# Optimization experiments

Measured on AMD Instinct MI355X. Metric: run time of the kernel, lower is better.

## Reference

```python
import jax, jax.numpy as jnp
import numpy as np

N = 8192        # num_nodes
H = 128         # h_dim
E = 131072      # num edges (avg degree 16)
NREL = 90       # num relations
NB = 8          # num_bases (block-diagonal decomposition)
SI = H // NB    # block size 16


def setup_inputs() -> dict:
    key = jax.random.key(0)
    ks = jax.random.split(key, 24)
    sc = 0.01
    n = lambda k, shape, s=sc: jax.random.normal(k, shape, dtype=jnp.float32) * s
    return {
        'node_ids': jnp.arange(N, dtype=jnp.int32),
        'src': jax.random.randint(ks[0], (E,), 0, N, dtype=jnp.int32),
        'dst': jax.random.randint(ks[1], (E,), 0, N, dtype=jnp.int32),
        'etypes': jax.random.randint(ks[2], (E,), 0, NREL, dtype=jnp.int32),
        'norm': jax.random.uniform(ks[3], (E, 1), dtype=jnp.float32),
        'eps': jax.random.normal(ks[4], (N, H), dtype=jnp.float32),
        # input embedding layer
        'embedding': n(ks[5], (N, H)),
        # RelGraphConv layer 0 ('bdd'): per-relation block-diag weights, self-loop, bias
        'W0': n(ks[6], (NREL, NB, SI, SI)),
        'loop0': n(ks[7], (H, H)),
        'b0': jnp.zeros((H,), jnp.float32),
        # RelGraphConv layer 1
        'W1': n(ks[8], (NREL, NB, SI, SI)),
        'loop1': n(ks[9], (H, H)),
        'b1': jnp.zeros((H,), jnp.float32),
        # z_layer: Linear(H, 2H)  (weights stored as (in, out))
        'Wz': n(ks[10], (H, 2 * H)),
        'bz': jnp.zeros((2 * H,), jnp.float32),
        # inter_layer (UpdateLayer): Linear(H, H) + h_bias
        'Wi': n(ks[11], (H, H)),
        'bi': jnp.zeros((H,), jnp.float32),
        'hbi': jnp.zeros((H,), jnp.float32),
        # output_layer (second UpdateLayer)
        'Wo': n(ks[12], (H, H)),
        'bo': jnp.zeros((H,), jnp.float32),
        'hbo': jnp.zeros((H,), jnp.float32),
    }


def _rgcn_bdd(h, W, loop_w, bias, src, dst, etypes, norm, act):
    # gather src features, split into NB blocks of size SI
    x = h[src].reshape(-1, NB, SI)                       # [E, NB, SI]
    Wg = W[etypes]                                       # [E, NB, SI, SI] per-edge relation block weights
    msg = jnp.einsum('ebi,ebio->ebo', x, Wg).reshape(-1, H) * norm  # [E, H]
    agg = jax.ops.segment_sum(msg, dst, num_segments=N)  # scatter-add to dst
    out = agg + bias + h @ loop_w                        # self-loop + bias
    return act(out) if act is not None else out


def reference(node_ids, src, dst, etypes, norm, eps, embedding,
              W0, loop0, b0, W1, loop1, b1,
              Wz, bz, Wi, bi, hbi, Wo, bo, hbo):
    # input layer: embedding lookup; saved as input_embed
    x0 = embedding[node_ids]                             # [N, H]
    h = _rgcn_bdd(x0, W0, loop0, b0, src, dst, etypes, norm, jax.nn.relu)
    h = _rgcn_bdd(h, W1, loop1, b1, src, dst, etypes, norm, None)
    # VAE head: z ~ N(mean, exp(log_std))
    zml = h @ Wz + bz                                    # [N, 2H]
    z_mean, z_log_std = jnp.split(zml, 2, axis=-1)
    z = z_mean + jnp.exp(z_log_std) * eps                # reparameterized sample
    # decode 1: outer-product reconstruction + fused update
    R = z @ z.T                                          # [N, N]
    h = R @ (z @ Wi + bi) + R @ x0 + hbi
    # decode 2
    R2 = h @ h.T                                         # [N, N]
    out = R2 @ (h @ Wo + bo) + R2 @ x0 + hbo
    return out
```

## Files before the change

### kernel.cpp

```cpp
#include <hip/hip_runtime.h>
#include <hip/hip_bf16.h>
#include <math.h>

#define Hdim 128
#define NBq 8
#define SIq 16
#define LDP 136
#define SKX 64

typedef __attribute__((ext_vector_type(8))) short short8x;
typedef __attribute__((ext_vector_type(8))) _Float16 half8x;
typedef __attribute__((ext_vector_type(4))) float f32x4;
typedef __attribute__((ext_vector_type(4))) unsigned short ushort4x;
typedef __attribute__((ext_vector_type(2))) _Float16 half2x;

__device__ inline unsigned short f2b(float f) {
  unsigned int u = __float_as_uint(f);
  return (unsigned short)((u + 0x7fffu + ((u >> 16) & 1u)) >> 16);
}
__device__ inline unsigned int pack2(float lo, float hi) {
  return (unsigned int)f2b(lo) | ((unsigned int)f2b(hi) << 16);
}
__device__ inline unsigned short f2h(float f) {
  _Float16 h = (_Float16)f;
  unsigned short u;
  __builtin_memcpy(&u, &h, 2);
  return u;
}
__device__ inline half2x u2h(unsigned int u) {
  union { unsigned int u; half2x h; } v;
  v.u = u;
  return v.h;
}
__device__ inline float b2f(unsigned short u) {
  return __uint_as_float(((unsigned int)u) << 16);
}

__global__ __launch_bounds__(256) void k_pre(
    const float* __restrict__ emb, const int* __restrict__ ids, float* __restrict__ x0,
    unsigned short* __restrict__ x0h, unsigned short* __restrict__ x0t, int Nn,
    const float* __restrict__ W0, unsigned short* __restrict__ Wt0,
    const float* __restrict__ W1, unsigned short* __restrict__ Wt1, int w0elems,
    const float* __restrict__ l0, const float* __restrict__ l1,
    const float* __restrict__ Wi, const float* __restrict__ Wo, const float* __restrict__ Wz,
    unsigned short* __restrict__ l0t, unsigned short* __restrict__ l1t,
    unsigned short* __restrict__ Wit, unsigned short* __restrict__ Wot,
    unsigned short* __restrict__ Wzt,
    const int* __restrict__ dst, int* __restrict__ cnt, int E,
    int b1, int b2, int b3) {
  int bx = blockIdx.x, t = threadIdx.x;
  if (bx < b1) {
    int idx = bx * 256 + t;
    int n = idx >> 5, c4 = idx & 31;
    int s = ids[n];
    float4 v = ((const float4*)emb)[(size_t)s * 32 + c4];
    ((float4*)x0)[(size_t)n * 32 + c4] = v;
    ushort4x h;
    h.x = f2h(v.x); h.y = f2h(v.y); h.z = f2h(v.z); h.w = f2h(v.w);
    ((ushort4x*)x0h)[(size_t)n * 32 + c4] = h;
    int c0 = c4 * 4;
    x0t[(size_t)(c0 + 0) * Nn + n] = h.x;
    x0t[(size_t)(c0 + 1) * Nn + n] = h.y;
    x0t[(size_t)(c0 + 2) * Nn + n] = h.z;
    x0t[(size_t)(c0 + 3) * Nn + n] = h.w;
  } else if (bx < b2) {
    int idx = (bx - b1) * 256 + t;
    const float* W = (idx < w0elems) ? W0 : W1;
    unsigned short* Wt = (idx < w0elems) ? Wt0 : Wt1;
    int local = (idx < w0elems) ? idx : idx - w0elems;
    int rb = local >> 8, io = local & 255;
    int i = io >> 4, o = io & 15;
    Wt[(size_t)rb * 256 + o * 16 + i] = f2h(W[(size_t)rb * 256 + i * 16 + o]);
  } else if (bx < b3) {
    int idx = (bx - b2) * 256 + t;
    if (idx < 65536) {
      int w = idx >> 14, local = idx & 16383;
      const float* in = (w == 0) ? l0 : (w == 1) ? l1 : (w == 2) ? Wi : Wo;
      unsigned short* out = (w == 0) ? l0t : (w == 1) ? l1t : (w == 2) ? Wit : Wot;
      int n = local >> 7, k = local & 127;
      out[local] = f2b(in[k * 128 + n]);
    } else {
      int local = idx - 65536;
      int n = local >> 7, k = local & 127;
      Wzt[local] = f2b(Wz[k * 256 + n]);
    }
  } else {
    int e = (bx - b3) * 256 + t;
    if (e < E) atomicAdd(&cnt[dst[e]], 1);
  }
}

__global__ __launch_bounds__(1024) void k_scan(const int* __restrict__ cnt,
                                               int* __restrict__ off,
                                               int* __restrict__ cur, int N, int E) {
  __shared__ int part[1024];
  int t = threadIdx.x;
  int ipt = N / 1024;
  int base = t * ipt;
  int loc[8];
  int s = 0;
  for (int i = 0; i < ipt; ++i) { loc[i] = s; s += cnt[base + i]; }
  part[t] = s;
  __syncthreads();
  for (int d = 1; d < 1024; d <<= 1) {
    int v = part[t];
    int add = (t >= d) ? part[t - d] : 0;
    __syncthreads();
    part[t] = v + add;
    __syncthreads();
  }
  int pre = (t == 0) ? 0 : part[t - 1];
  for (int i = 0; i < ipt; ++i) {
    int o = pre + loc[i];
    off[base + i] = o;
    cur[base + i] = o;
  }
  if (t == 0) off[N] = E;
}

__global__ void k_scatter(const int* __restrict__ src, const int* __restrict__ dst,
                          const int* __restrict__ et, const float* __restrict__ norm,
                          int* __restrict__ cur, int4* __restrict__ pedge, int E) {
  int e = blockIdx.x * blockDim.x + threadIdx.x;
  if (e >= E) return;
  int p = atomicAdd(&cur[dst[e]], 1);
  pedge[p] = make_int4(src[e], et[e], __float_as_int(norm[e]), 0);
}

__global__ __launch_bounds__(128) void k_edge(
    const unsigned short* __restrict__ xh, const unsigned short* __restrict__ Wt,
    const int* __restrict__ off, const int4* __restrict__ pedge,
    float* __restrict__ agg) {
  int n = blockIdx.x;
  int f = threadIdx.x;
  int b = f >> 4, o = f & 15;
  int j0 = off[n], j1 = off[n + 1];
  float acc = 0.f;
#pragma unroll 2
  for (int j = j0; j < j1; ++j) {
    int4 meta = pedge[j];
    int s = meta.x;
    int r = meta.y;
    float nv = __int_as_float(meta.z);
    const uint4* xp = (const uint4*)(xh + (size_t)s * Hdim + b * SIq);
    const uint4* wp = (const uint4*)(Wt + ((size_t)r * NBq + b) * 256 + o * SIq);
    uint4 xa = xp[0], xc = xp[1];
    uint4 wa = wp[0], wc = wp[1];
#if __has_builtin(__builtin_amdgcn_fdot2)
    float d0 = 0.f, d1 = 0.f;
    d0 = __builtin_amdgcn_fdot2(u2h(xa.x), u2h(wa.x), d0, false);
    d1 = __builtin_amdgcn_fdot2(u2h(xa.y), u2h(wa.y), d1, false);
    d0 = __builtin_amdgcn_fdot2(u2h(xa.z), u2h(wa.z), d0, false);
    d1 = __builtin_amdgcn_fdot2(u2h(xa.w), u2h(wa.w), d1, false);
    d0 = __builtin_amdgcn_fdot2(u2h(xc.x), u2h(wc.x), d0, false);
    d1 = __builtin_amdgcn_fdot2(u2h(xc.y), u2h(wc.y), d1, false);
    d0 = __builtin_amdgcn_fdot2(u2h(xc.z), u2h(wc.z), d0, false);
    d1 = __builtin_amdgcn_fdot2(u2h(xc.w), u2h(wc.w), d1, false);
    acc = fmaf(d0 + d1, nv, acc);
#else
    float d = 0.f;
    unsigned int xu[8] = {xa.x, xa.y, xa.z, xa.w, xc.x, xc.y, xc.z, xc.w};
    unsigned int wu[8] = {wa.x, wa.y, wa.z, wa.w, wc.x, wc.y, wc.z, wc.w};
#pragma unroll
    for (int k = 0; k < 8; ++k) {
      half2x xv = u2h(xu[k]), wv = u2h(wu[k]);
      d += (float)xv.x * (float)wv.x + (float)xv.y * (float)wv.y;
    }
    acc = fmaf(d, nv, acc);
#endif
  }
  agg[(size_t)n * Hdim + f] = acc;
}

__global__ __launch_bounds__(256) void k_bgemm(
    const float* __restrict__ A, const unsigned short* __restrict__ Bt,
    float* __restrict__ C,
    const float* __restrict__ addm, const float* __restrict__ bias,
    int M, int Nc, int relu, unsigned short* __restrict__ Ch) {
  __shared__ unsigned short Al[32][136];
  __shared__ unsigned short Bl[64][136];
  int t = threadIdx.x;
  int bm = blockIdx.x * 32, bn = blockIdx.y * 64;
  {
    int r = t >> 3, c0 = (t & 7) << 4;
    const float4* ap = (const float4*)(A + (size_t)(bm + r) * Hdim + c0);
    float4 a0 = ap[0], a1 = ap[1], a2 = ap[2], a3 = ap[3];
    uint4 p0 = { pack2(a0.x, a0.y), pack2(a0.z, a0.w), pack2(a1.x, a1.y), pack2(a1.z, a1.w) };
    uint4 p1 = { pack2(a2.x, a2.y), pack2(a2.z, a2.w), pack2(a3.x, a3.y), pack2(a3.z, a3.w) };
    *(uint4*)&Al[r][c0]     = p0;
    *(uint4*)&Al[r][c0 + 8] = p1;
  }
  {
    int n = t >> 2, k0 = (t & 3) << 5;
    const uint4* bp = (const uint4*)(Bt + (size_t)(bn + n) * Hdim + k0);
    uint4 b0 = bp[0], b1 = bp[1], b2 = bp[2], b3 = bp[3];
    *(uint4*)&Bl[n][k0]      = b0;
    *(uint4*)&Bl[n][k0 + 8]  = b1;
    *(uint4*)&Bl[n][k0 + 16] = b2;
    *(uint4*)&Bl[n][k0 + 24] = b3;
  }
  __syncthreads();
  int wv = t >> 6, ln = t & 63;
  int mt = wv & 1;
  int nt0 = (wv >> 1) << 1;
  int lm = ln & 15, lk = ln >> 4;
  f32x4 acc0 = {0.f, 0.f, 0.f, 0.f}, acc1 = {0.f, 0.f, 0.f, 0.f};
#pragma unroll
  for (int ks = 0; ks < 4; ++ks) {
    short8x af = *(const short8x*)&Al[mt * 16 + lm][ks * 32 + lk * 8];
    short8x bf0 = *(const short8x*)&Bl[nt0 * 16 + lm][ks * 32 + lk * 8];
    short8x bf1 = *(const short8x*)&Bl[(nt0 + 1) * 16 + lm][ks * 32 + lk * 8];
    acc0 = __builtin_amdgcn_mfma_f32_16x16x32_bf16(af, bf0, acc0, 0, 0, 0);
    acc1 = __builtin_amdgcn_mfma_f32_16x16x32_bf16(af, bf1, acc1, 0, 0, 0);
  }
  int gcol0 = bn + nt0 * 16 + lm;
  int gcol1 = gcol0 + 16;
  float b0v = bias ? bias[gcol0] : 0.f;
  float b1v = bias ? bias[gcol1] : 0.f;
#pragma unroll
  for (int reg = 0; reg < 4; ++reg) {
    int grow = bm + mt * 16 + lk * 4 + reg;
    size_t o0 = (size_t)grow * Nc + gcol0;
    size_t o1 = (size_t)grow * Nc + gcol1;
    float v0 = acc0[reg] + b0v;
    float v1 = acc1[reg] + b1v;
    if (addm) { v0 += addm[o0]; v1 += addm[o1]; }
    if (relu) { v0 = fmaxf(v0, 0.f); v1 = fmaxf(v1, 0.f); }
    C[o0] = v0;
    C[o1] = v1;
    if (Ch) { Ch[o0] = f2h(v0); Ch[o1] = f2h(v1); }
  }
}

__global__ __launch_bounds__(256) void k_bgemm_z(
    const float* __restrict__ A, const unsigned short* __restrict__ Wzt,
    const float* __restrict__ bz, const float* __restrict__ eps,
    float* __restrict__ Z, int M, int Nn,
    unsigned short* __restrict__ Zth, float* __restrict__ gz) {
  __shared__ unsigned short Al[32][136];
  __shared__ unsigned short Bm[64][136];
  __shared__ unsigned short Bl[64][136];
  int t = threadIdx.x;
  int bm = blockIdx.x * 32, bn = blockIdx.y * 64;
  if (gz && blockIdx.x == 0 && blockIdx.y == 0 && t < 64)
    ((float4*)gz)[t] = make_float4(0.f, 0.f, 0.f, 0.f);
  {
    int r = t >> 3, c0 = (t & 7) << 4;
    const float4* ap = (const float4*)(A + (size_t)(bm + r) * Hdim + c0);
    float4 a0 = ap[0], a1 = ap[1], a2 = ap[2], a3 = ap[3];
    uint4 p0 = { pack2(a0.x, a0.y), pack2(a0.z, a0.w), pack2(a1.x, a1.y), pack2(a1.z, a1.w) };
    uint4 p1 = { pack2(a2.x, a2.y), pack2(a2.z, a2.w), pack2(a3.x, a3.y), pack2(a3.z, a3.w) };
    *(uint4*)&Al[r][c0]     = p0;
    *(uint4*)&Al[r][c0 + 8] = p1;
  }
  {
    int n = t >> 2, k0 = (t & 3) << 5;
    const uint4* mp = (const uint4*)(Wzt + (size_t)(bn + n) * Hdim + k0);
    const uint4* lp = (const uint4*)(Wzt + (size_t)(bn + 128 + n) * Hdim + k0);
    uint4 m0 = mp[0], m1 = mp[1], m2 = mp[2], m3 = mp[3];
    uint4 l0 = lp[0], l1 = lp[1], l2 = lp[2], l3 = lp[3];
    *(uint4*)&Bm[n][k0]      = m0; *(uint4*)&Bm[n][k0 + 8]  = m1;
    *(uint4*)&Bm[n][k0 + 16] = m2; *(uint4*)&Bm[n][k0 + 24] = m3;
    *(uint4*)&Bl[n][k0]      = l0; *(uint4*)&Bl[n][k0 + 8]  = l1;
    *(uint4*)&Bl[n][k0 + 16] = l2; *(uint4*)&Bl[n][k0 + 24] = l3;
  }
  __syncthreads();
  int wv = t >> 6, ln = t & 63;
  int mt = wv & 1;
  int nt0 = (wv >> 1) << 1;
  int lm = ln & 15, lk = ln >> 4;
  f32x4 am0 = {0,0,0,0}, am1 = {0,0,0,0}, al0 = {0,0,0,0}, al1 = {0,0,0,0};
#pragma unroll
  for (int ks = 0; ks < 4; ++ks) {
    short8x af = *(const short8x*)&Al[mt * 16 + lm][ks * 32 + lk * 8];
    short8x bm0 = *(const short8x*)&Bm[nt0 * 16 + lm][ks * 32 + lk * 8];
    short8x bm1 = *(const short8x*)&Bm[(nt0 + 1) * 16 + lm][ks * 32 + lk * 8];
    short8x bl0 = *(const short8x*)&Bl[nt0 * 16 + lm][ks * 32 + lk * 8];
    short8x bl1 = *(const short8x*)&Bl[(nt0 + 1) * 16 + lm][ks * 32 + lk * 8];
    am0 = __builtin_amdgcn_mfma_f32_16x16x32_bf16(af, bm0, am0, 0, 0, 0);
    am1 = __builtin_amdgcn_mfma_f32_16x16x32_bf16(af, bm1, am1, 0, 0, 0);
    al0 = __builtin_amdgcn_mfma_f32_16x16x32_bf16(af, bl0, al0, 0, 0, 0);
    al1 = __builtin_amdgcn_mfma_f32_16x16x32_bf16(af, bl1, al1, 0, 0, 0);
  }
  int gcol0 = bn + nt0 * 16 + lm;
  int gcol1 = gcol0 + 16;
  float bm0v = bz[gcol0], bm1v = bz[gcol1];
  float bl0v = bz[128 + gcol0], bl1v = bz[128 + gcol1];
#pragma unroll
  for (int reg = 0; reg < 4; ++reg) {
    int grow = bm + mt * 16 + lk * 4 + reg;
    size_t o0 = (size_t)grow * Hdim + gcol0;
    size_t o1 = (size_t)grow * Hdim + gcol1;
    float v0 = am0[reg] + bm0v + expf(al0[reg] + bl0v) * eps[o0];
    float v1 = am1[reg] + bm1v + expf(al1[reg] + bl1v) * eps[o1];
    Z[o0] = v0;
    Z[o1] = v1;
    Zth[(size_t)gcol0 * Nn + grow] = f2h(v0);
    Zth[(size_t)gcol1 * Nn + grow] = f2h(v1);
  }
}

__global__ __launch_bounds__(256) void k_xty2m(
    const unsigned short* __restrict__ Zt, const unsigned short* __restrict__ X0t,
    float* __restrict__ part, float* __restrict__ s1, float* __restrict__ cx0, int N) {
  int kc = blockIdx.x, yt = blockIdx.y;
  int t = threadIdx.x;
  int KC = N / SKX;
  int k0 = kc * KC;
  if (yt == 4) {
    int c = t & 127;
    const unsigned short* row = ((t >> 7) ? X0t : Zt) + (size_t)c * N + k0;
    float acc = 0.f;
    for (int i = 0; i < KC; i += 8) {
      uint4 v = *(const uint4*)(row + i);
      half2x a0 = u2h(v.x), a1 = u2h(v.y), a2 = u2h(v.z), a3 = u2h(v.w);
      acc += (float)a0.x + (float)a0.y + (float)a1.x + (float)a1.y
           + (float)a2.x + (float)a2.y + (float)a3.x + (float)a3.y;
    }
    atomicAdd(((t >> 7) ? cx0 : s1) + c, acc);
    return;
  }
  __shared__ unsigned short Asl[128][72];
  __shared__ unsigned short Bsl[64][72];
  int wv = t >> 6, ln = t & 63, lm = ln & 15, lk = ln >> 4;
  f32x4 acc[8];
#pragma unroll
  for (int i = 0; i < 8; ++i) acc[i] = (f32x4){0.f, 0.f, 0.f, 0.f};
  for (int ch = 0; ch < KC; ch += 64) {
    {
      int r = t >> 1, s = (t & 1) * 32;
      const uint4* gp = (const uint4*)(Zt + (size_t)r * N + k0 + ch + s);
      uint4 v0 = gp[0], v1 = gp[1], v2 = gp[2], v3 = gp[3];
      *(uint4*)&Asl[r][s]      = v0;
      *(uint4*)&Asl[r][s + 8]  = v1;
      *(uint4*)&Asl[r][s + 16] = v2;
      *(uint4*)&Asl[r][s + 24] = v3;
    }
    if (t < 128) {
      int n = t >> 1, s = (t & 1) * 32;
      int yn = yt * 64 + n;
      const unsigned short* Sb = (yn < 128) ? (Zt + (size_t)yn * N)
                                            : (X0t + (size_t)(yn - 128) * N);
      const uint4* gp = (const uint4*)(Sb + k0 + ch + s);
      uint4 v0 = gp[0], v1 = gp[1], v2 = gp[2], v3 = gp[3];
      *(uint4*)&Bsl[n][s]      = v0;
      *(uint4*)&Bsl[n][s + 8]  = v1;
      *(uint4*)&Bsl[n][s + 16] = v2;
      *(uint4*)&Bsl[n][s + 24] = v3;
    }
    __syncthreads();
#pragma unroll
    for (int ks = 0; ks < 2; ++ks) {
      half8x bf = *(const half8x*)&Bsl[wv * 16 + lm][ks * 32 + lk * 8];
#pragma unroll
      for (int mi = 0; mi < 8; ++mi) {
        half8x af = *(const half8x*)&Asl[mi * 16 + lm][ks * 32 + lk * 8];
        acc[mi] = __builtin_amdgcn_mfma_f32_16x16x32_f16(af, bf, acc[mi], 0, 0, 0);
      }
    }
    __syncthreads();
  }
  int gcol = yt * 64 + wv * 16 + lm;
  float* pb = part + (size_t)kc * (128 * 256) + gcol;
#pragma unroll
  for (int mi = 0; mi < 8; ++mi)
#pragma unroll
    for (int rg = 0; rg < 4; ++rg)
      pb[(size_t)(mi * 16 + lk * 4 + rg) * 256] = acc[mi][rg];
}

__global__ __launch_bounds__(256) void k_red(const float* __restrict__ part,
                                             float* __restrict__ SP) {
  int idx = blockIdx.x * 256 + threadIdx.x;
  float a = 0.f;
#pragma unroll 8
  for (int s = 0; s < SKX; ++s) a += part[(size_t)s * 32768 + idx];
  SP[idx] = a;
}

__device__ inline void stage_f32(unsigned short* dst, const float* __restrict__ src,
                                 int ldF, int t) {
#pragma unroll
  for (int it = 0; it < 2; ++it) {
    int id = it * 1024 + t; int row = id >> 4, ch = id & 15;
    const float4* gp = (const float4*)(src + (size_t)row * ldF) + ch * 2;
    float4 u = gp[0], v = gp[1];
    uint4 pk = { pack2(u.x, u.y), pack2(u.z, u.w), pack2(v.x, v.y), pack2(v.z, v.w) };
    *(uint4*)&dst[row * LDP + ch * 8] = pk;
  }
}
__device__ inline void stage_b16(unsigned short* dst, const unsigned short* __restrict__ src,
                                 int t) {
#pragma unroll
  for (int it = 0; it < 2; ++it) {
    int id = it * 1024 + t; int row = id >> 4, ch = id & 15;
    *(uint4*)&dst[row * LDP + ch * 8] = ((const uint4*)(src + (size_t)row * 128))[ch];
  }
}
__device__ inline void mm128(const unsigned short* A, const unsigned short* B,
                             f32x4 (&Cc)[2][2], int wr, int wc, int lm, int lk) {
#pragma unroll
  for (int ks = 0; ks < 4; ++ks) {
    short8x af0 = *(const short8x*)&A[(wr * 32 + lm) * LDP + ks * 32 + lk * 8];
    short8x af1 = *(const short8x*)&A[(wr * 32 + 16 + lm) * LDP + ks * 32 + lk * 8];
    short8x bf0 = *(const short8x*)&B[(wc * 32 + lm) * LDP + ks * 32 + lk * 8];
    short8x bf1 = *(const short8x*)&B[(wc * 32 + 16 + lm) * LDP + ks * 32 + lk * 8];
    Cc[0][0] = __builtin_amdgcn_mfma_f32_16x16x32_bf16(af0, bf0, Cc[0][0], 0, 0, 0);
    Cc[0][1] = __builtin_amdgcn_mfma_f32_16x16x32_bf16(af0, bf1, Cc[0][1], 0, 0, 0);
    Cc[1][0] = __builtin_amdgcn_mfma_f32_16x16x32_bf16(af1, bf0, Cc[1][0], 0, 0, 0);
    Cc[1][1] = __builtin_amdgcn_mfma_f32_16x16x32_bf16(af1, bf1, Cc[1][1], 0, 0, 0);
  }
}
#define ZEROC {                                           \
  _Pragma("unroll") for (int mi = 0; mi < 2; ++mi)        \
  _Pragma("unroll") for (int ni = 0; ni < 2; ++ni)        \
    C[mi][ni] = (f32x4){0.f, 0.f, 0.f, 0.f}; }

__global__ __launch_bounds__(1024) void k_fix(
    const float* __restrict__ SP, const float* __restrict__ s1g,
    const float* __restrict__ cx0g,
    const unsigned short* __restrict__ Wit, const unsigned short* __restrict__ Wot,
    const float* __restrict__ bi, const float* __restrict__ hbi,
    const float* __restrict__ bo, const float* __restrict__ hbo,
    unsigned short* __restrict__ G12t, float* __restrict__ bvec, float Nf) {
  __shared__ unsigned short T0[128 * LDP];
  __shared__ unsigned short T1[128 * LDP];
  __shared__ unsigned short T2[128 * LDP];
  __shared__ unsigned short T3[128 * LDP];
  __shared__ float s1l[128], tl[128], s2l[128], cxl[128], bil[128], bol[128], hl[128];
  int t = threadIdx.x;
  int wv = t >> 6, ln = t & 63, lm = ln & 15, lk = ln >> 4;
  int wr = wv >> 2, wc = wv & 3;
  if (t < 128) {
    s1l[t] = s1g[t]; cxl[t] = cx0g[t]; bil[t] = bi[t]; bol[t] = bo[t]; hl[t] = hbi[t];
  }
  stage_f32(T0, SP, 256, t);
  stage_b16(T1, Wit, t);
  __syncthreads();
  f32x4 C[2][2];
  ZEROC; mm128(T0, T1, C, wr, wc, lm, lk);
#pragma unroll
  for (int mi = 0; mi < 2; ++mi)
#pragma unroll
// ... 89 lines not shown
  for (int ni = 0; ni < 2; ++ni) {
    int gcol = wc * 32 + ni * 16 + lm;
    int g0 = wr * 32 + mi * 16 + lk * 4;
#pragma unroll
    for (int rg = 0; rg < 4; ++rg) {
      int grow = g0 + rg;
      g2v[mi][ni][rg] = C[mi][ni][rg] + s2l[grow] * bol[gcol]
                      + b2f(T0[grow * LDP + gcol]);
    }
  }
  __syncthreads();
#pragma unroll
  for (int mi = 0; mi < 2; ++mi)
#pragma unroll
  for (int ni = 0; ni < 2; ++ni) {
    int gcol = wc * 32 + ni * 16 + lm;
    int g0 = wr * 32 + mi * 16 + lk * 4;
    ushort4x pk;
#pragma unroll
    for (int rg = 0; rg < 4; ++rg) pk[rg] = f2b(g2v[mi][ni][rg]);
    *(ushort4x*)&T0[gcol * LDP + g0] = pk;
  }
  __syncthreads();
  {
    int row = t >> 3, seg = t & 7;
    const unsigned short* gr = T0 + row * LDP + seg * 16;
    float a2 = 0.f;
#pragma unroll
    for (int i = 0; i < 16; ++i) a2 += hl[seg * 16 + i] * b2f(gr[i]);
    a2 += __shfl_xor(a2, 1);
    a2 += __shfl_xor(a2, 2);
    a2 += __shfl_xor(a2, 4);
    if (seg == 0) bvec[row] = a2 + hbo[row];
  }
  ZEROC; mm128(T2, T0, C, wr, wc, lm, lk);
#pragma unroll
  for (int mi = 0; mi < 2; ++mi)
#pragma unroll
  for (int ni = 0; ni < 2; ++ni) {
    int gcol = wc * 32 + ni * 16 + lm;
    int g0 = wr * 32 + mi * 16 + lk * 4;
    ushort4x pk;
#pragma unroll
    for (int rg = 0; rg < 4; ++rg) pk[rg] = f2b(C[mi][ni][rg]);
    *(ushort4x*)&T1[gcol * LDP + g0] = pk;
  }
  __syncthreads();
#pragma unroll
  for (int it = 0; it < 2; ++it) {
    int id = it * 1024 + t; int row = id >> 4, ch = (id & 15) * 8;
    *(uint4*)&G12t[row * 128 + ch] = *(uint4*)&T1[row * LDP + ch];
  }
}

extern "C" void kernel_launch(void* const* d_in, const int* in_sizes, int n_in,
                              void* d_out, int out_size, void* d_ws, size_t ws_size,
                              hipStream_t stream) {
  const int*   node_ids = (const int*)d_in[0];
  const int*   src      = (const int*)d_in[1];
  const int*   dst      = (const int*)d_in[2];
  const int*   et       = (const int*)d_in[3];
  const float* norm     = (const float*)d_in[4];
  const float* eps      = (const float*)d_in[5];
  const float* emb      = (const float*)d_in[6];
  const float* W0       = (const float*)d_in[7];
  const float* loop0    = (const float*)d_in[8];
  const float* b0       = (const float*)d_in[9];
  const float* W1       = (const float*)d_in[10];
  const float* loop1    = (const float*)d_in[11];
  const float* b1       = (const float*)d_in[12];
  const float* Wz       = (const float*)d_in[13];
  const float* bz       = (const float*)d_in[14];
  const float* Wi       = (const float*)d_in[15];
  const float* bi       = (const float*)d_in[16];
  const float* hbi      = (const float*)d_in[17];
  const float* Wo       = (const float*)d_in[18];
  const float* bo       = (const float*)d_in[19];
  const float* hbo      = (const float*)d_in[20];
  float* out = (float*)d_out;

  const int N  = in_sizes[0];
  const int E  = in_sizes[1];
  const int RB = in_sizes[7] / (SIq * SIq);

  char* ws = (char*)d_ws;
  const size_t MB = 1u << 20;
  const size_t KB = 1u << 10;
  float* X0   = (float*)(ws + 0 * MB);
  float* B1p  = (float*)(ws + 4 * MB);
  float* B2p  = (float*)(ws + 8 * MB);
  float* AGG  = (float*)(ws + 12 * MB);
  float* part = (float*)(ws + 8 * MB);
  float* SPb  = (float*)(ws + 16 * MB);
  float* s1p  = SPb + 32768;
  float* cx0p = SPb + 32896;
  unsigned short* G12t = (unsigned short*)(ws + 16 * MB + 576 * KB);
  float* bvec = (float*)(ws + 16 * MB + 640 * KB);
  int*   offp = (int*)(ws + 17 * MB);
  int*   curp = (int*)(ws + 17 * MB + 128 * KB);
  int*   cntp = (int*)(ws + 17 * MB + 256 * KB);
  int4*  pedge = (int4*)(ws + 18 * MB);
  unsigned short* Wt0 = (unsigned short*)(ws + 20 * MB);
  unsigned short* Wt1 = (unsigned short*)(ws + 20 * MB + 512 * KB);
  unsigned short* l0t = (unsigned short*)(ws + 21 * MB);
  unsigned short* l1t = (unsigned short*)(ws + 21 * MB + 64 * KB);
  unsigned short* Wit = (unsigned short*)(ws + 21 * MB + 128 * KB);
  unsigned short* Wot = (unsigned short*)(ws + 21 * MB + 192 * KB);
  unsigned short* Wzt = (unsigned short*)(ws + 21 * MB + 256 * KB);
  unsigned short* X0H = (unsigned short*)(ws + 22 * MB);
  unsigned short* B1H = (unsigned short*)(ws + 24 * MB);
  unsigned short* Ztc = (unsigned short*)(ws + 26 * MB);
  unsigned short* X0t = (unsigned short*)(ws + 28 * MB);

  dim3 blk(256);

  const int w0elems = RB * 256;
  const int gB   = (N * 32) / 256;
  const int wtbB = (2 * w0elems + 255) / 256;
  const int wttB = 98304 / 256;
  const int histB = (E + 255) / 256;
  const int b1s = gB, b2s = gB + wtbB, b3s = gB + wtbB + wttB;
  hipMemsetAsync(cntp, 0, (size_t)N * sizeof(int), stream);
  k_pre<<<dim3(b3s + histB), blk, 0, stream>>>(
      emb, node_ids, X0, X0H, X0t, N, W0, Wt0, W1, Wt1, w0elems,
      loop0, loop1, Wi, Wo, Wz, l0t, l1t, Wit, Wot, Wzt,
      dst, cntp, E, b1s, b2s, b3s);
  k_scan<<<dim3(1), dim3(1024), 0, stream>>>(cntp, offp, curp, N, E);
  k_scatter<<<dim3((E + 255) / 256), blk, 0, stream>>>(src, dst, et, norm, curp, pedge, E);

  k_edge<<<dim3(N), dim3(128), 0, stream>>>(X0H, Wt0, offp, pedge, AGG);
  k_bgemm<<<dim3(N / 32, 2), blk, 0, stream>>>(X0, l0t, B1p, AGG, b0, N, Hdim, 1, B1H);
  k_edge<<<dim3(N), dim3(128), 0, stream>>>(B1H, Wt1, offp, pedge, AGG);
  k_bgemm<<<dim3(N / 32, 2), blk, 0, stream>>>(B1p, l1t, B2p, AGG, b1, N, Hdim, 0, nullptr);
  k_bgemm_z<<<dim3(N / 32, 2), blk, 0, stream>>>(B2p, Wzt, bz, eps, B1p, N, N, Ztc, s1p);
  k_xty2m<<<dim3(SKX, 5), blk, 0, stream>>>(Ztc, X0t, part, s1p, cx0p, N);
  k_red<<<dim3(128), blk, 0, stream>>>(part, SPb);
  k_fix<<<dim3(1), dim3(1024), 0, stream>>>(SPb, s1p, cx0p, Wit, Wot, bi, hbi, bo, hbo,
                                            G12t, bvec, (float)N);
  k_bgemm<<<dim3(N / 32, 2), blk, 0, stream>>>(B1p, G12t, out, nullptr, bvec, N, Hdim, 0, nullptr);
}
```

Measured before the change: 253.2 us.

## Drop transposed fp16 copies of Z and X0; transpose in shared memory instead

Removes the strided transposed writes of Z (in k_bgemm_z) and X0 (in k_pre) to separate column-major fp16 buffers. k_xty2m now reads row-major fp32 Z and fp16 X0 directly, converts to fp16 in registers and transposes while storing into shared memory. The column-sum path now also reads row-major with a per-element loop. This trades uncoalesced scattered global writes for scalar shared-memory transposed stores, possible bank conflicts, and reading fp32 Z (twice the bytes) in the Gram kernel. It also drops the trailing barrier by moving the sync before the shared stores.

Measured after the change: 261.1 us. 1.03x slower.

```diff
diff --git a/kernel.cpp b/kernel.cpp
--- a/kernel.cpp
+++ b/kernel.cpp
@@ -27,6 +27,11 @@
   __builtin_memcpy(&u, &h, 2);
   return u;
 }
+__device__ inline float h2f(unsigned short u) {
+  _Float16 h;
+  __builtin_memcpy(&h, &u, 2);
+  return (float)h;
+}
 __device__ inline half2x u2h(unsigned int u) {
   union { unsigned int u; half2x h; } v;
   v.u = u;
@@ -38,7 +43,7 @@
 
 __global__ __launch_bounds__(256) void k_pre(
     const float* __restrict__ emb, const int* __restrict__ ids, float* __restrict__ x0,
-    unsigned short* __restrict__ x0h, unsigned short* __restrict__ x0t, int Nn,
+    unsigned short* __restrict__ x0h,
     const float* __restrict__ W0, unsigned short* __restrict__ Wt0,
     const float* __restrict__ W1, unsigned short* __restrict__ Wt1, int w0elems,
     const float* __restrict__ l0, const float* __restrict__ l1,
@@ -58,11 +63,6 @@
     ushort4x h;
     h.x = f2h(v.x); h.y = f2h(v.y); h.z = f2h(v.z); h.w = f2h(v.w);
     ((ushort4x*)x0h)[(size_t)n * 32 + c4] = h;
-    int c0 = c4 * 4;
-    x0t[(size_t)(c0 + 0) * Nn + n] = h.x;
-    x0t[(size_t)(c0 + 1) * Nn + n] = h.y;
-    x0t[(size_t)(c0 + 2) * Nn + n] = h.z;
-    x0t[(size_t)(c0 + 3) * Nn + n] = h.w;
   } else if (bx < b2) {
     int idx = (bx - b1) * 256 + t;
     const float* W = (idx < w0elems) ? W0 : W1;
@@ -235,8 +235,7 @@
 __global__ __launch_bounds__(256) void k_bgemm_z(
     const float* __restrict__ A, const unsigned short* __restrict__ Wzt,
     const float* __restrict__ bz, const float* __restrict__ eps,
-    float* __restrict__ Z, int M, int Nn,
-    unsigned short* __restrict__ Zth, float* __restrict__ gz) {
+    float* __restrict__ Z, int M, float* __restrict__ gz) {
   __shared__ unsigned short Al[32][136];
   __shared__ unsigned short Bm[64][136];
   __shared__ unsigned short Bl[64][136];
@@ -291,17 +290,13 @@
     int grow = bm + mt * 16 + lk * 4 + reg;
     size_t o0 = (size_t)grow * Hdim + gcol0;
     size_t o1 = (size_t)grow * Hdim + gcol1;
-    float v0 = am0[reg] + bm0v + expf(al0[reg] + bl0v) * eps[o0];
-    float v1 = am1[reg] + bm1v + expf(al1[reg] + bl1v) * eps[o1];
-    Z[o0] = v0;
-    Z[o1] = v1;
-    Zth[(size_t)gcol0 * Nn + grow] = f2h(v0);
-    Zth[(size_t)gcol1 * Nn + grow] = f2h(v1);
+    Z[o0] = am0[reg] + bm0v + expf(al0[reg] + bl0v) * eps[o0];
+    Z[o1] = am1[reg] + bm1v + expf(al1[reg] + bl1v) * eps[o1];
   }
 }
 
 __global__ __launch_bounds__(256) void k_xty2m(
-    const unsigned short* __restrict__ Zt, const unsigned short* __restrict__ X0t,
+    const float* __restrict__ Z, const unsigned short* __restrict__ X0h,
     float* __restrict__ part, float* __restrict__ s1, float* __restrict__ cx0, int N) {
   int kc = blockIdx.x, yt = blockIdx.y;
   int t = threadIdx.x;
@@ -309,45 +304,63 @@
   int k0 = kc * KC;
   if (yt == 4) {
     int c = t & 127;
-    const unsigned short* row = ((t >> 7) ? X0t : Zt) + (size_t)c * N + k0;
     float acc = 0.f;
-    for (int i = 0; i < KC; i += 8) {
-      uint4 v = *(const uint4*)(row + i);
-      half2x a0 = u2h(v.x), a1 = u2h(v.y), a2 = u2h(v.z), a3 = u2h(v.w);
-      acc += (float)a0.x + (float)a0.y + (float)a1.x + (float)a1.y
-           + (float)a2.x + (float)a2.y + (float)a3.x + (float)a3.y;
-    }
-    atomicAdd(((t >> 7) ? cx0 : s1) + c, acc);
+    if (t >> 7) {
+      for (int i = 0; i < KC; ++i)
+        acc += h2f(X0h[(size_t)(k0 + i) * Hdim + c]);
+      atomicAdd(cx0 + c, acc);
+    } else {
+      for (int i = 0; i < KC; ++i)
+        acc += Z[(size_t)(k0 + i) * Hdim + c];
+      atomicAdd(s1 + c, acc);
+    }
     return;
   }
   __shared__ unsigned short Asl[128][72];
   __shared__ unsigned short Bsl[64][72];
   int wv = t >> 6, ln = t & 63, lm = ln & 15, lk = ln >> 4;
+  int sn = t & 63, sq = t >> 6;
   f32x4 acc[8];
 #pragma unroll
   for (int i = 0; i < 8; ++i) acc[i] = (f32x4){0.f, 0.f, 0.f, 0.f};
   for (int ch = 0; ch < KC; ch += 64) {
+    int nrow = k0 + ch + sn;
+    unsigned short atmp[32];
     {
-      int r = t >> 1, s = (t & 1) * 32;
-      const uint4* gp = (const uint4*)(Zt + (size_t)r * N + k0 + ch + s);
-      uint4 v0 = gp[0], v1 = gp[1], v2 = gp[2], v3 = gp[3];
-      *(uint4*)&Asl[r][s]      = v0;
-      *(uint4*)&Asl[r][s + 8]  = v1;
-      *(uint4*)&Asl[r][s + 16] = v2;
-      *(uint4*)&Asl[r][s + 24] = v3;
-    }
-    if (t < 128) {
-      int n = t >> 1, s = (t & 1) * 32;
-      int yn = yt * 64 + n;
-      const unsigned short* Sb = (yn < 128) ? (Zt + (size_t)yn * N)
-                                            : (X0t + (size_t)(yn - 128) * N);
-      const uint4* gp = (const uint4*)(Sb + k0 + ch + s);
-      uint4 v0 = gp[0], v1 = gp[1], v2 = gp[2], v3 = gp[3];
-      *(uint4*)&Bsl[n][s]      = v0;
-      *(uint4*)&Bsl[n][s + 8]  = v1;
-      *(uint4*)&Bsl[n][s + 16] = v2;
-      *(uint4*)&Bsl[n][s + 24] = v3;
-    }
+      const float4* zr = (const float4*)(Z + (size_t)nrow * Hdim + sq * 32);
+#pragma unroll
+      for (int u = 0; u < 8; ++u) {
+        float4 v = zr[u];
+        atmp[u * 4 + 0] = f2h(v.x);
+        atmp[u * 4 + 1] = f2h(v.y);
+        atmp[u * 4 + 2] = f2h(v.z);
+        atmp[u * 4 + 3] = f2h(v.w);
+      }
+    }
+    unsigned short btmp[16];
+    if (yt < 2) {
+      const float4* zr = (const float4*)(Z + (size_t)nrow * Hdim + yt * 64 + sq * 16);
+#pragma unroll
+      for (int u = 0; u < 4; ++u) {
+        float4 v = zr[u];
+        btmp[u * 4 + 0] = f2h(v.x);
+        btmp[u * 4 + 1] = f2h(v.y);
+        btmp[u * 4 + 2] = f2h(v.z);
+        btmp[u * 4 + 3] = f2h(v.w);
+      }
+    } else {
+      const uint4* xr = (const uint4*)(X0h + (size_t)nrow * Hdim + (yt - 2) * 64 + sq * 16);
+#pragma unroll
+      for (int u = 0; u < 2; ++u) {
+        uint4 v = xr[u];
+        __builtin_memcpy(&btmp[u * 8], &v, 16);
+      }
+    }
+    __syncthreads();
+#pragma unroll
+    for (int q = 0; q < 32; ++q) Asl[sq * 32 + q][sn] = atmp[q];
+#pragma unroll
+    for (int q = 0; q < 16; ++q) Bsl[sq * 16 + q][sn] = btmp[q];
     __syncthreads();
 #pragma unroll
     for (int ks = 0; ks < 2; ++ks) {
@@ -358,7 +371,6 @@
         acc[mi] = __builtin_amdgcn_mfma_f32_16x16x32_f16(af, bf, acc[mi], 0, 0, 0);
       }
     }
-    __syncthreads();
   }
   int gcol = yt * 64 + wv * 16 + lm;
   float* pb = part + (size_t)kc * (128 * 256) + gcol;
@@ -641,8 +653,6 @@
   unsigned short* Wzt = (unsigned short*)(ws + 21 * MB + 256 * KB);
   unsigned short* X0H = (unsigned short*)(ws + 22 * MB);
   unsigned short* B1H = (unsigned short*)(ws + 24 * MB);
-  unsigned short* Ztc = (unsigned short*)(ws + 26 * MB);
-  unsigned short* X0t = (unsigned short*)(ws + 28 * MB);
 
   dim3 blk(256);
 
@@ -654,7 +664,7 @@
   const int b1s = gB, b2s = gB + wtbB, b3s = gB + wtbB + wttB;
   hipMemsetAsync(cntp, 0, (size_t)N * sizeof(int), stream);
   k_pre<<<dim3(b3s + histB), blk, 0, stream>>>(
-      emb, node_ids, X0, X0H, X0t, N, W0, Wt0, W1, Wt1, w0elems,
+      emb, node_ids, X0, X0H, W0, Wt0, W1, Wt1, w0elems,
       loop0, loop1, Wi, Wo, Wz, l0t, l1t, Wit, Wot, Wzt,
       dst, cntp, E, b1s, b2s, b3s);
   k_scan<<<dim3(1), dim3(1024), 0, stream>>>(cntp, offp, curp, N, E);
@@ -664,8 +674,8 @@
   k_bgemm<<<dim3(N / 32, 2), blk, 0, stream>>>(X0, l0t, B1p, AGG, b0, N, Hdim, 1, B1H);
   k_edge<<<dim3(N), dim3(128), 0, stream>>>(B1H, Wt1, offp, pedge, AGG);
   k_bgemm<<<dim3(N / 32, 2), blk, 0, stream>>>(B1p, l1t, B2p, AGG, b1, N, Hdim, 0, nullptr);
-  k_bgemm_z<<<dim3(N / 32, 2), blk, 0, stream>>>(B2p, Wzt, bz, eps, B1p, N, N, Ztc, s1p);
-  k_xty2m<<<dim3(SKX, 5), blk, 0, stream>>>(Ztc, X0t, part, s1p, cx0p, N);
+  k_bgemm_z<<<dim3(N / 32, 2), blk, 0, stream>>>(B2p, Wzt, bz, eps, B1p, N, s1p);
+  k_xty2m<<<dim3(SKX, 5), blk, 0, stream>>>(B1p, X0H, part, s1p, cx0p, N);
   k_red<<<dim3(128), blk, 0, stream>>>(part, SPb);
   k_fix<<<dim3(1), dim3(1024), 0, stream>>>(SPb, s1p, cx0p, Wit, Wot, bi, hbi, bo, hbo,
                                             G12t, bvec, (float)N);
```

## Group edges by relation and compute messages with MFMA, then segment-reduce

Applied to the files above, without the earlier changes.

Edges are now bucketed by relation type via a second histogram and scan, so 16-edge tiles of the same relation can run the block-diagonal transform as a 16x16x32 f16 MFMA. Each message is scaled by its norm and written as fp16 into a per-edge buffer indexed by its dst-sorted slot. A separate kernel then sums each node's contiguous messages. This replaces the per-edge scalar dot-product loop, which reloaded relation weights for every edge. In exchange it adds an extra E×H fp16 round trip through global memory, more atomics in the scatter stage, and fp16 rounding of every message.

New measurement: 538.6 us. 2.13x slower.

```diff
diff --git a/kernel.cpp b/kernel.cpp
--- a/kernel.cpp
+++ b/kernel.cpp
@@ -46,7 +46,8 @@
     unsigned short* __restrict__ l0t, unsigned short* __restrict__ l1t,
     unsigned short* __restrict__ Wit, unsigned short* __restrict__ Wot,
     unsigned short* __restrict__ Wzt,
-    const int* __restrict__ dst, int* __restrict__ cnt, int E,
+    const int* __restrict__ dst, const int* __restrict__ et,
+    int* __restrict__ cnt, int* __restrict__ ehist, int E,
     int b1, int b2, int b3) {
   int bx = blockIdx.x, t = threadIdx.x;
   if (bx < b1) {
@@ -86,13 +87,20 @@
     }
   } else {
     int e = (bx - b3) * 256 + t;
-    if (e < E) atomicAdd(&cnt[dst[e]], 1);
+    if (e < E) {
+      atomicAdd(&cnt[dst[e]], 1);
+      atomicAdd(&ehist[et[e]], 1);
+    }
   }
 }
 
 __global__ __launch_bounds__(1024) void k_scan(const int* __restrict__ cnt,
                                                int* __restrict__ off,
-                                               int* __restrict__ cur, int N, int E) {
+                                               int* __restrict__ cur, int N, int E,
+                                               const int* __restrict__ ehist,
+                                               int* __restrict__ eoff,
+                                               int* __restrict__ ecur,
+                                               int* __restrict__ tileoff, int NREL) {
   __shared__ int part[1024];
   int t = threadIdx.x;
   int ipt = N / 1024;
@@ -115,61 +123,97 @@
     off[base + i] = o;
     cur[base + i] = o;
   }
-  if (t == 0) off[N] = E;
+  if (t == 0) {
+    off[N] = E;
+    int run = 0, trun = 0;
+    for (int r = 0; r < NREL; ++r) {
+      eoff[r] = run; ecur[r] = run; tileoff[r] = trun;
+      int c = ehist[r];
+      run += c; trun += (c + 15) >> 4;
+    }
+    eoff[NREL] = run; tileoff[NREL] = trun;
+  }
 }
 
 __global__ void k_scatter(const int* __restrict__ src, const int* __restrict__ dst,
                           const int* __restrict__ et, const float* __restrict__ norm,
-                          int* __restrict__ cur, int4* __restrict__ pedge, int E) {
+                          int* __restrict__ cur, int* __restrict__ ecur,
+                          int4* __restrict__ pedge, int E) {
   int e = blockIdx.x * blockDim.x + threadIdx.x;
   if (e >= E) return;
   int p = atomicAdd(&cur[dst[e]], 1);
-  pedge[p] = make_int4(src[e], et[e], __float_as_int(norm[e]), 0);
-}
-
-__global__ __launch_bounds__(128) void k_edge(
-    const unsigned short* __restrict__ xh, const unsigned short* __restrict__ Wt,
-    const int* __restrict__ off, const int4* __restrict__ pedge,
-    float* __restrict__ agg) {
-  int n = blockIdx.x;
-  int f = threadIdx.x;
-  int b = f >> 4, o = f & 15;
+  int q = atomicAdd(&ecur[et[e]], 1);
+  pedge[q] = make_int4(src[e], p, __float_as_int(norm[e]), 0);
+}
+
+__global__ __launch_bounds__(256) void k_msg(
+    const unsigned short* __restrict__ xh,
+    const unsigned short* __restrict__ Wt,
+    const int4* __restrict__ em,
+    const int* __restrict__ eoff, const int* __restrict__ tileoff,
+    unsigned short* __restrict__ msg, int NREL) {
+  __shared__ int toff[128];
+  int t = threadIdx.x;
+  if (t <= NREL) toff[t] = tileoff[t];
+  __syncthreads();
+  int ntiles = toff[NREL];
+  int l = t & 63, w = t >> 6;
+  int lm = l & 15, lg = l >> 4;
+#pragma unroll 1
+  for (int tt = 0; tt < 4; ++tt) {
+    int tile = blockIdx.x * 4 + tt;
+    if (tile >= ntiles) break;
+    int lo = 0, hi = NREL - 1;
+    while (lo < hi) { int mid = (lo + hi + 1) >> 1; if (toff[mid] <= tile) lo = mid; else hi = mid - 1; }
+    int r = lo;
+    int estart = eoff[r] + (tile - toff[r]) * 16;
+    int count = eoff[r + 1] - estart;
+    if (count > 16) count = 16;
+    int4 meta = em[estart + (lm < count ? lm : 0)];
+    int msrc = meta.x;
+#pragma unroll
+    for (int bb = 0; bb < 2; ++bb) {
+      int b = w + bb * 4;
+      half8x af;
+#pragma unroll
+      for (int j = 0; j < 8; ++j) af[j] = (_Float16)0.f;
+      if (lg < 2 && lm < count)
+        af = *(const half8x*)(xh + (size_t)msrc * Hdim + b * 16 + lg * 8);
+      int gg = lg & 1;
+      half8x bf = *(const half8x*)(Wt + ((size_t)r * NBq + b) * 256 + lm * 16 + gg * 8);
+      f32x4 d = {0.f, 0.f, 0.f, 0.f};
+      d = __builtin_amdgcn_mfma_f32_16x16x32_f16(af, bf, d, 0, 0, 0);
+#pragma unroll
+      for (int reg = 0; reg < 4; ++reg) {
+        int m2 = lg * 4 + reg;
+        int slot = __shfl(meta.y, m2);
+        int nb2  = __shfl(meta.z, m2);
+        if (m2 < count)
+          msg[(size_t)slot * Hdim + b * 16 + lm] = f2h(d[reg] * __int_as_float(nb2));
+      }
+    }
+  }
+}
+
+__global__ __launch_bounds__(256) void k_seg(const unsigned short* __restrict__ msg,
+                                             const int* __restrict__ off,
+                                             float* __restrict__ agg) {
+  int n = blockIdx.x * 16 + (threadIdx.x >> 4);
+  int c8 = (threadIdx.x & 15) * 8;
   int j0 = off[n], j1 = off[n + 1];
-  float acc = 0.f;
-#pragma unroll 2
+  float acc[8] = {0.f, 0.f, 0.f, 0.f, 0.f, 0.f, 0.f, 0.f};
   for (int j = j0; j < j1; ++j) {
-    int4 meta = pedge[j];
-    int s = meta.x;
-    int r = meta.y;
-    float nv = __int_as_float(meta.z);
-    const uint4* xp = (const uint4*)(xh + (size_t)s * Hdim + b * SIq);
-    const uint4* wp = (const uint4*)(Wt + ((size_t)r * NBq + b) * 256 + o * SIq);
-    uint4 xa = xp[0], xc = xp[1];
-    uint4 wa = wp[0], wc = wp[1];
-#if __has_builtin(__builtin_amdgcn_fdot2)
-    float d0 = 0.f, d1 = 0.f;
-    d0 = __builtin_amdgcn_fdot2(u2h(xa.x), u2h(wa.x), d0, false);
-    d1 = __builtin_amdgcn_fdot2(u2h(xa.y), u2h(wa.y), d1, false);
-    d0 = __builtin_amdgcn_fdot2(u2h(xa.z), u2h(wa.z), d0, false);
-    d1 = __builtin_amdgcn_fdot2(u2h(xa.w), u2h(wa.w), d1, false);
-    d0 = __builtin_amdgcn_fdot2(u2h(xc.x), u2h(wc.x), d0, false);
-    d1 = __builtin_amdgcn_fdot2(u2h(xc.y), u2h(wc.y), d1, false);
-    d0 = __builtin_amdgcn_fdot2(u2h(xc.z), u2h(wc.z), d0, false);
-    d1 = __builtin_amdgcn_fdot2(u2h(xc.w), u2h(wc.w), d1, false);
-    acc = fmaf(d0 + d1, nv, acc);
-#else
-    float d = 0.f;
-    unsigned int xu[8] = {xa.x, xa.y, xa.z, xa.w, xc.x, xc.y, xc.z, xc.w};
-    unsigned int wu[8] = {wa.x, wa.y, wa.z, wa.w, wc.x, wc.y, wc.z, wc.w};
-#pragma unroll
-    for (int k = 0; k < 8; ++k) {
-      half2x xv = u2h(xu[k]), wv = u2h(wu[k]);
-      d += (float)xv.x * (float)wv.x + (float)xv.y * (float)wv.y;
-    }
-    acc = fmaf(d, nv, acc);
-#endif
-  }
-  agg[(size_t)n * Hdim + f] = acc;
+    uint4 v = *(const uint4*)(msg + (size_t)j * Hdim + c8);
+    half2x h0 = u2h(v.x), h1 = u2h(v.y), h2 = u2h(v.z), h3 = u2h(v.w);
+    acc[0] += (float)h0.x; acc[1] += (float)h0.y;
+    acc[2] += (float)h1.x; acc[3] += (float)h1.y;
+    acc[4] += (float)h2.x; acc[5] += (float)h2.y;
+    acc[6] += (float)h3.x; acc[7] += (float)h3.y;
+  }
+  float4 o0 = {acc[0], acc[1], acc[2], acc[3]};
+  float4 o1 = {acc[4], acc[5], acc[6], acc[7]};
+  *(float4*)(agg + (size_t)n * Hdim + c8)     = o0;
+  *(float4*)(agg + (size_t)n * Hdim + c8 + 4) = o1;
 }
 
 __global__ __launch_bounds__(256) void k_bgemm(
@@ -614,6 +658,7 @@
   const int N  = in_sizes[0];
   const int E  = in_sizes[1];
   const int RB = in_sizes[7] / (SIq * SIq);
+  const int NREL = RB / NBq;
 
   char* ws = (char*)d_ws;
   const size_t MB = 1u << 20;
@@ -631,6 +676,10 @@
   int*   offp = (int*)(ws + 17 * MB);
   int*   curp = (int*)(ws + 17 * MB + 128 * KB);
   int*   cntp = (int*)(ws + 17 * MB + 256 * KB);
+  int*   ehist = cntp + N;
+  int*   eoffp = (int*)(ws + 17 * MB + 320 * KB);
+  int*   ecurp = (int*)(ws + 17 * MB + 328 * KB);
+  int*   tilep = (int*)(ws + 17 * MB + 336 * KB);
   int4*  pedge = (int4*)(ws + 18 * MB);
   unsigned short* Wt0 = (unsigned short*)(ws + 20 * MB);
   unsigned short* Wt1 = (unsigned short*)(ws + 20 * MB + 512 * KB);
@@ -643,6 +692,7 @@
   unsigned short* B1H = (unsigned short*)(ws + 24 * MB);
   unsigned short* Ztc = (unsigned short*)(ws + 26 * MB);
   unsigned short* X0t = (unsigned short*)(ws + 28 * MB);
+  unsigned short* msg = (unsigned short*)(ws + 32 * MB);
 
   dim3 blk(256);
 
@@ -652,17 +702,24 @@
   const int wttB = 98304 / 256;
   const int histB = (E + 255) / 256;
   const int b1s = gB, b2s = gB + wtbB, b3s = gB + wtbB + wttB;
-  hipMemsetAsync(cntp, 0, (size_t)N * sizeof(int), stream);
+  hipMemsetAsync(cntp, 0, (size_t)(N + 128) * sizeof(int), stream);
   k_pre<<<dim3(b3s + histB), blk, 0, stream>>>(
       emb, node_ids, X0, X0H, X0t, N, W0, Wt0, W1, Wt1, w0elems,
       loop0, loop1, Wi, Wo, Wz, l0t, l1t, Wit, Wot, Wzt,
-      dst, cntp, E, b1s, b2s, b3s);
-  k_scan<<<dim3(1), dim3(1024), 0, stream>>>(cntp, offp, curp, N, E);
-  k_scatter<<<dim3((E + 255) / 256), blk, 0, stream>>>(src, dst, et, norm, curp, pedge, E);
-
-  k_edge<<<dim3(N), dim3(128), 0, stream>>>(X0H, Wt0, offp, pedge, AGG);
+      dst, et, cntp, ehist, E, b1s, b2s, b3s);
+  k_scan<<<dim3(1), dim3(1024), 0, stream>>>(cntp, offp, curp, N, E,
+                                             ehist, eoffp, ecurp, tilep, NREL);
+  k_scatter<<<dim3((E + 255) / 256), blk, 0, stream>>>(src, dst, et, norm, curp,
+                                                       ecurp, pedge, E);
+
+  const int maxTiles = E / 16 + NREL;
+  const int msgB = (maxTiles + 3) / 4;
+
+  k_msg<<<dim3(msgB), blk, 0, stream>>>(X0H, Wt0, pedge, eoffp, tilep, msg, NREL);
+  k_seg<<<dim3(N / 16), blk, 0, stream>>>(msg, offp, AGG);
   k_bgemm<<<dim3(N / 32, 2), blk, 0, stream>>>(X0, l0t, B1p, AGG, b0, N, Hdim, 1, B1H);
-  k_edge<<<dim3(N), dim3(128), 0, stream>>>(B1H, Wt1, offp, pedge, AGG);
+  k_msg<<<dim3(msgB), blk, 0, stream>>>(B1H, Wt1, pedge, eoffp, tilep, msg, NREL);
+  k_seg<<<dim3(N / 16), blk, 0, stream>>>(msg, offp, AGG);
   k_bgemm<<<dim3(N / 32, 2), blk, 0, stream>>>(B1p, l1t, B2p, AGG, b1, N, Hdim, 0, nullptr);
   k_bgemm_z<<<dim3(N / 32, 2), blk, 0, stream>>>(B2p, Wzt, bz, eps, B1p, N, N, Ztc, s1p);
   k_xty2m<<<dim3(SKX, 5), blk, 0, stream>>>(Ztc, X0t, part, s1p, cx0p, N);
```

## Fuse edge message aggregation into self-loop GEMM kernel

Applied to the files above, without the earlier changes.

Merges the per-node edge gather/aggregate kernel into the self-loop bf16 MFMA GEMM, so each 32x64 tile computes its aggregation into shared memory and adds it in the epilogue. This removes two kernel launches per layer and the global round-trip of the AGG buffer. In exchange the grid shrinks from N blocks of 128 threads to N/32 x 2 blocks, each looping over 8 nodes per wave serially, which may lower the parallelism available for hiding gather latency.

New measurement: 291.9 us. 1.15x slower.

```diff
diff --git a/kernel.cpp b/kernel.cpp
--- a/kernel.cpp
+++ b/kernel.cpp
@@ -127,49 +127,114 @@
   pedge[p] = make_int4(src[e], et[e], __float_as_int(norm[e]), 0);
 }
 
-__global__ __launch_bounds__(128) void k_edge(
+__global__ __launch_bounds__(256) void k_bgemm_e(
+    const float* __restrict__ A, const unsigned short* __restrict__ Bt,
+    float* __restrict__ C, const float* __restrict__ bias,
+    int M, int relu, unsigned short* __restrict__ Ch,
     const unsigned short* __restrict__ xh, const unsigned short* __restrict__ Wt,
-    const int* __restrict__ off, const int4* __restrict__ pedge,
-    float* __restrict__ agg) {
-  int n = blockIdx.x;
-  int f = threadIdx.x;
-  int b = f >> 4, o = f & 15;
-  int j0 = off[n], j1 = off[n + 1];
-  float acc = 0.f;
+    const int* __restrict__ off, const int4* __restrict__ pedge) {
+  __shared__ unsigned short Al[32][136];
+  __shared__ unsigned short Bl[64][136];
+  __shared__ float aggL[32][64];
+  int t = threadIdx.x;
+  int bm = blockIdx.x * 32, bn = blockIdx.y * 64;
+  {
+    int r = t >> 3, c0 = (t & 7) << 4;
+    const float4* ap = (const float4*)(A + (size_t)(bm + r) * Hdim + c0);
+    float4 a0 = ap[0], a1 = ap[1], a2 = ap[2], a3 = ap[3];
+    uint4 p0 = { pack2(a0.x, a0.y), pack2(a0.z, a0.w), pack2(a1.x, a1.y), pack2(a1.z, a1.w) };
+    uint4 p1 = { pack2(a2.x, a2.y), pack2(a2.z, a2.w), pack2(a3.x, a3.y), pack2(a3.z, a3.w) };
+    *(uint4*)&Al[r][c0]     = p0;
+    *(uint4*)&Al[r][c0 + 8] = p1;
+  }
+  {
+    int n = t >> 2, k0 = (t & 3) << 5;
+    const uint4* bp = (const uint4*)(Bt + (size_t)(bn + n) * Hdim + k0);
+    uint4 b0 = bp[0], b1 = bp[1], b2 = bp[2], b3 = bp[3];
+    *(uint4*)&Bl[n][k0]      = b0;
+    *(uint4*)&Bl[n][k0 + 8]  = b1;
+    *(uint4*)&Bl[n][k0 + 16] = b2;
+    *(uint4*)&Bl[n][k0 + 24] = b3;
+  }
+  {
+    int lane = t & 63, wavei = t >> 6;
+    int gcol = bn + lane;
+    int b = gcol >> 4, o = gcol & 15;
+#pragma unroll 1
+    for (int p = 0; p < 8; ++p) {
+      int nl = p * 4 + wavei;
+      int n = bm + nl;
+      int j0 = off[n], j1 = off[n + 1];
+      float acc = 0.f;
 #pragma unroll 2
-  for (int j = j0; j < j1; ++j) {
-    int4 meta = pedge[j];
-    int s = meta.x;
-    int r = meta.y;
-    float nv = __int_as_float(meta.z);
-    const uint4* xp = (const uint4*)(xh + (size_t)s * Hdim + b * SIq);
-    const uint4* wp = (const uint4*)(Wt + ((size_t)r * NBq + b) * 256 + o * SIq);
-    uint4 xa = xp[0], xc = xp[1];
-    uint4 wa = wp[0], wc = wp[1];
+      for (int j = j0; j < j1; ++j) {
+        int4 meta = pedge[j];
+        int s = meta.x;
+        int r = meta.y;
+        float nv = __int_as_float(meta.z);
+        const uint4* xp = (const uint4*)(xh + (size_t)s * Hdim + b * SIq);
+        const uint4* wp = (const uint4*)(Wt + ((size_t)r * NBq + b) * 256 + o * SIq);
+        uint4 xa = xp[0], xc = xp[1];
+        uint4 wa = wp[0], wc = wp[1];
 #if __has_builtin(__builtin_amdgcn_fdot2)
-    float d0 = 0.f, d1 = 0.f;
-    d0 = __builtin_amdgcn_fdot2(u2h(xa.x), u2h(wa.x), d0, false);
-    d1 = __builtin_amdgcn_fdot2(u2h(xa.y), u2h(wa.y), d1, false);
-    d0 = __builtin_amdgcn_fdot2(u2h(xa.z), u2h(wa.z), d0, false);
-    d1 = __builtin_amdgcn_fdot2(u2h(xa.w), u2h(wa.w), d1, false);
-    d0 = __builtin_amdgcn_fdot2(u2h(xc.x), u2h(wc.x), d0, false);
-    d1 = __builtin_amdgcn_fdot2(u2h(xc.y), u2h(wc.y), d1, false);
-    d0 = __builtin_amdgcn_fdot2(u2h(xc.z), u2h(wc.z), d0, false);
-    d1 = __builtin_amdgcn_fdot2(u2h(xc.w), u2h(wc.w), d1, false);
-    acc = fmaf(d0 + d1, nv, acc);
+        float d0 = 0.f, d1 = 0.f;
+        d0 = __builtin_amdgcn_fdot2(u2h(xa.x), u2h(wa.x), d0, false);
+        d1 = __builtin_amdgcn_fdot2(u2h(xa.y), u2h(wa.y), d1, false);
+        d0 = __builtin_amdgcn_fdot2(u2h(xa.z), u2h(wa.z), d0, false);
+        d1 = __builtin_amdgcn_fdot2(u2h(xa.w), u2h(wa.w), d1, false);
+        d0 = __builtin_amdgcn_fdot2(u2h(xc.x), u2h(wc.x), d0, false);
+        d1 = __builtin_amdgcn_fdot2(u2h(xc.y), u2h(wc.y), d1, false);
+        d0 = __builtin_amdgcn_fdot2(u2h(xc.z), u2h(wc.z), d0, false);
+        d1 = __builtin_amdgcn_fdot2(u2h(xc.w), u2h(wc.w), d1, false);
+        acc = fmaf(d0 + d1, nv, acc);
 #else
-    float d = 0.f;
-    unsigned int xu[8] = {xa.x, xa.y, xa.z, xa.w, xc.x, xc.y, xc.z, xc.w};
-    unsigned int wu[8] = {wa.x, wa.y, wa.z, wa.w, wc.x, wc.y, wc.z, wc.w};
-#pragma unroll
-    for (int k = 0; k < 8; ++k) {
-      half2x xv = u2h(xu[k]), wv = u2h(wu[k]);
-      d += (float)xv.x * (float)wv.x + (float)xv.y * (float)wv.y;
-    }
-    acc = fmaf(d, nv, acc);
+        float d = 0.f;
+        unsigned int xu[8] = {xa.x, xa.y, xa.z, xa.w, xc.x, xc.y, xc.z, xc.w};
+        unsigned int wu[8] = {wa.x, wa.y, wa.z, wa.w, wc.x, wc.y, wc.z, wc.w};
+#pragma unroll
+        for (int k = 0; k < 8; ++k) {
+          half2x xv = u2h(xu[k]), wv = u2h(wu[k]);
+          d += (float)xv.x * (float)wv.x + (float)xv.y * (float)wv.y;
+        }
+        acc = fmaf(d, nv, acc);
 #endif
-  }
-  agg[(size_t)n * Hdim + f] = acc;
+      }
+      aggL[nl][lane] = acc;
+    }
+  }
+  __syncthreads();
+  int wv = t >> 6, ln = t & 63;
+  int mt = wv & 1;
+  int nt0 = (wv >> 1) << 1;
+  int lm = ln & 15, lk = ln >> 4;
+  f32x4 acc0 = {0.f, 0.f, 0.f, 0.f}, acc1 = {0.f, 0.f, 0.f, 0.f};
+#pragma unroll
+  for (int ks = 0; ks < 4; ++ks) {
+    short8x af = *(const short8x*)&Al[mt * 16 + lm][ks * 32 + lk * 8];
+    short8x bf0 = *(const short8x*)&Bl[nt0 * 16 + lm][ks * 32 + lk * 8];
+    short8x bf1 = *(const short8x*)&Bl[(nt0 + 1) * 16 + lm][ks * 32 + lk * 8];
+    acc0 = __builtin_amdgcn_mfma_f32_16x16x32_bf16(af, bf0, acc0, 0, 0, 0);
+    acc1 = __builtin_amdgcn_mfma_f32_16x16x32_bf16(af, bf1, acc1, 0, 0, 0);
+  }
+  int lc0 = nt0 * 16 + lm;
+  int lc1 = lc0 + 16;
+  int gcol0 = bn + lc0;
+  int gcol1 = bn + lc1;
+  float b0v = bias ? bias[gcol0] : 0.f;
+  float b1v = bias ? bias[gcol1] : 0.f;
+#pragma unroll
+  for (int reg = 0; reg < 4; ++reg) {
+    int lrow = mt * 16 + lk * 4 + reg;
+    int grow = bm + lrow;
+    size_t o0 = (size_t)grow * Hdim + gcol0;
+    size_t o1 = (size_t)grow * Hdim + gcol1;
+    float v0 = acc0[reg] + b0v + aggL[lrow][lc0];
+    float v1 = acc1[reg] + b1v + aggL[lrow][lc1];
+    if (relu) { v0 = fmaxf(v0, 0.f); v1 = fmaxf(v1, 0.f); }
+    C[o0] = v0;
+    C[o1] = v1;
+    if (Ch) { Ch[o0] = f2h(v0); Ch[o1] = f2h(v1); }
+  }
 }
 
 __global__ __launch_bounds__(256) void k_bgemm(
@@ -621,7 +686,6 @@
   float* X0   = (float*)(ws + 0 * MB);
   float* B1p  = (float*)(ws + 4 * MB);
   float* B2p  = (float*)(ws + 8 * MB);
-  float* AGG  = (float*)(ws + 12 * MB);
   float* part = (float*)(ws + 8 * MB);
   float* SPb  = (float*)(ws + 16 * MB);
   float* s1p  = SPb + 32768;
@@ -660,10 +724,10 @@
   k_scan<<<dim3(1), dim3(1024), 0, stream>>>(cntp, offp, curp, N, E);
   k_scatter<<<dim3((E + 255) / 256), blk, 0, stream>>>(src, dst, et, norm, curp, pedge, E);
 
-  k_edge<<<dim3(N), dim3(128), 0, stream>>>(X0H, Wt0, offp, pedge, AGG);
-  k_bgemm<<<dim3(N / 32, 2), blk, 0, stream>>>(X0, l0t, B1p, AGG, b0, N, Hdim, 1, B1H);
-  k_edge<<<dim3(N), dim3(128), 0, stream>>>(B1H, Wt1, offp, pedge, AGG);
-  k_bgemm<<<dim3(N / 32, 2), blk, 0, stream>>>(B1p, l1t, B2p, AGG, b1, N, Hdim, 0, nullptr);
+  k_bgemm_e<<<dim3(N / 32, 2), blk, 0, stream>>>(X0, l0t, B1p, b0, N, 1, B1H,
+                                                 X0H, Wt0, offp, pedge);
+  k_bgemm_e<<<dim3(N / 32, 2), blk, 0, stream>>>(B1p, l1t, B2p, b1, N, 0, nullptr,
+                                                 B1H, Wt1, offp, pedge);
   k_bgemm_z<<<dim3(N / 32, 2), blk, 0, stream>>>(B2p, Wzt, bz, eps, B1p, N, N, Ztc, s1p);
   k_xty2m<<<dim3(SKX, 5), blk, 0, stream>>>(Ztc, X0t, part, s1p, cx0p, N);
   k_red<<<dim3(128), blk, 0, stream>>>(part, SPb);
```
